# Performance work log

Hardware: AMD Instinct MI355X
Metric: run time of the kernel (lower is better)

## Reference

```python
import jax, jax.numpy as jnp
import numpy as np

N = 50000      # nodes
E = 200000     # edges
IN = 768       # in_dim
HID = 256      # hidden_dim
OUT = 64       # out_dim
H = 4          # heads in conv1
R = 6          # n_relations
NEG = 0.2      # LeakyReLU negative slope (PyG default)
EPS = 1e-5     # LayerNorm eps


def layer_norm(h, g, b):
    mu = jnp.mean(h, axis=-1, keepdims=True)
    var = jnp.mean((h - mu) ** 2, axis=-1, keepdims=True)
    return (h - mu) * jax.lax.rsqrt(var + EPS) * g + b


def gat_layer(x, src, dst, W, a_src, a_dst, bias, heads, dh):
    # project: [N, heads, dh]
    h = (x @ W).reshape(-1, heads, dh)
    # per-node attention logits [N, heads]
    al_s = jnp.sum(h * a_src, axis=-1)
    al_d = jnp.sum(h * a_dst, axis=-1)
    # per-edge scores (edge j->i: source contributes al_s[j], target al_d[i])
    e = jax.nn.leaky_relu(al_s[src] + al_d[dst], NEG)  # [E, heads]
    # segment softmax over edges sharing the same destination node
    e_max = jax.ops.segment_max(e, dst, num_segments=N)        # [N, heads]
    ex = jnp.exp(e - e_max[dst])                               # [E, heads]
    denom = jax.ops.segment_sum(ex, dst, num_segments=N)       # [N, heads]
    alpha = ex / denom[dst]                                    # [E, heads]
    # weighted scatter-aggregate of source messages
    msg = h[src] * alpha[:, :, None]                            # [E, heads, dh]
    out = jax.ops.segment_sum(msg, dst, num_segments=N)        # [N, heads, dh]
    return out.reshape(-1, heads * dh) + bias


def setup_inputs() -> dict:
    key = jax.random.key(0)
    ks = jax.random.split(key, 16)
    s = 0.05  # keep attention logits tame
    return {
        "x": jax.random.normal(ks[0], (N, IN), jnp.float32),
        "edge_index": jax.random.randint(ks[1], (2, E), 0, N, dtype=jnp.int64),
        "edge_type": jax.random.randint(ks[2], (E,), 0, R, dtype=jnp.int64),
        "edge_emb": jax.random.normal(ks[3], (R, IN), jnp.float32) * s,
        "W1": jax.random.normal(ks[4], (IN, H * (HID // H)), jnp.float32) * s,
        "a_src1": jax.random.normal(ks[5], (H, HID // H), jnp.float32) * s,
        "a_dst1": jax.random.normal(ks[6], (H, HID // H), jnp.float32) * s,
        "b1": jnp.zeros((HID,), jnp.float32),
        "g1": jnp.ones((HID,), jnp.float32),
        "be1": jnp.zeros((HID,), jnp.float32),
        "W2": jax.random.normal(ks[7], (HID, OUT), jnp.float32) * s,
        "a_src2": jax.random.normal(ks[8], (1, OUT), jnp.float32) * s,
        "a_dst2": jax.random.normal(ks[9], (1, OUT), jnp.float32) * s,
        "b2": jnp.zeros((OUT,), jnp.float32),
        "g2": jnp.ones((OUT,), jnp.float32),
        "be2": jnp.zeros((OUT,), jnp.float32),
    }


def reference(x, edge_index, edge_type, edge_emb, W1, a_src1, a_dst1, b1, g1, be1,
              W2, a_src2, a_dst2, b2, g2, be2):
    src, dst = edge_index[0], edge_index[1]
    edge_feat = edge_emb[edge_type]                 # [E, IN]
    x_mod = x.at[src].set(x[src] + edge_feat)
    h = gat_layer(x_mod, src, dst, W1, a_src1, a_dst1, b1, H, HID // H)
    h = layer_norm(h, g1, be1)
    h = jax.nn.elu(h)                                # dropout off (inference)
    h = gat_layer(h, src, dst, W2, a_src2, a_dst2, b2, 1, OUT)
    h = layer_norm(h, g2, be2)
    return h
```

## Files before the change

kernel.cpp:

```cpp
#include <hip/hip_runtime.h>
#include <cstdint>
#include <cstddef>

#define NN 50000
#define NE 200000
#define IND 768
#define HID 256
#define OUTD 64
#define NB 196

typedef __bf16 bf16;
typedef __bf16 bf16x8 __attribute__((ext_vector_type(8)));
typedef __bf16 bf16x4 __attribute__((ext_vector_type(4)));
typedef float f32x4 __attribute__((ext_vector_type(4)));

__global__ __launch_bounds__(256) void k_edge_prep(const int* __restrict__ ei,
                                                   int* __restrict__ le, int* __restrict__ deg) {
  int e = blockIdx.x * 256 + threadIdx.x;
  if (e < NE) {
    atomicMax(&le[ei[e]], e);
    atomicAdd(&deg[ei[NE + e]], 1);
  }
}

__global__ __launch_bounds__(256) void k_eembz(const float* __restrict__ eemb,
                                               float* __restrict__ ez) {
  int i = blockIdx.x * 256 + threadIdx.x;
  if (i < 7 * IND) ez[i] = (i < 6 * IND) ? eemb[i] : 0.f;
}

__global__ __launch_bounds__(256) void k_prep_a(const float* __restrict__ x,
                                                const int* __restrict__ le,
                                                const int* __restrict__ et,
                                                const float* __restrict__ eembz,
                                                bf16* __restrict__ A1) {
  int idx = blockIdx.x * 256 + threadIdx.x;
  if (idx >= NN * (IND / 8)) return;
  int row = idx / (IND / 8);
  int c = (idx - row * (IND / 8)) * 8;
  int l = le[row];
  int e = (l >= 0) ? et[l] : 6;
  const float* px = x + (size_t)row * IND + c;
  const float* pe = eembz + (size_t)e * IND + c;
  float4 v0 = *(const float4*)px, v1 = *(const float4*)(px + 4);
  float4 e0 = *(const float4*)pe, e1 = *(const float4*)(pe + 4);
  bf16x8 o;
  o[0] = (bf16)(v0.x + e0.x); o[1] = (bf16)(v0.y + e0.y);
  o[2] = (bf16)(v0.z + e0.z); o[3] = (bf16)(v0.w + e0.w);
  o[4] = (bf16)(v1.x + e1.x); o[5] = (bf16)(v1.y + e1.y);
  o[6] = (bf16)(v1.z + e1.z); o[7] = (bf16)(v1.w + e1.w);
  *(bf16x8*)(A1 + (size_t)row * IND + c) = o;
}

__global__ __launch_bounds__(256) void k_scan_block(const int* __restrict__ deg,
                                                    int* __restrict__ excl, int* __restrict__ bsum) {
  __shared__ int sm[256];
  int tid = threadIdx.x;
  int i = blockIdx.x * 256 + tid;
  int v = (i < NN) ? deg[i] : 0;
  sm[tid] = v;
  __syncthreads();
#pragma unroll
  for (int off = 1; off < 256; off <<= 1) {
    int t = (tid >= off) ? sm[tid - off] : 0;
    __syncthreads();
    sm[tid] += t;
    __syncthreads();
  }
  if (i < NN) excl[i] = sm[tid] - v;
  if (tid == 255) bsum[blockIdx.x] = sm[255];
}

__global__ __launch_bounds__(256) void k_scan_partials(const int* __restrict__ bsum,
                                                       int* __restrict__ bbase) {
  __shared__ int sm[256];
  int tid = threadIdx.x;
  int v = (tid < NB) ? bsum[tid] : 0;
  sm[tid] = v;
  __syncthreads();
#pragma unroll
  for (int off = 1; off < 256; off <<= 1) {
    int t = (tid >= off) ? sm[tid - off] : 0;
    __syncthreads();
    sm[tid] += t;
    __syncthreads();
  }
  bbase[tid] = sm[tid] - v;
}

__global__ __launch_bounds__(256) void k_add_base(const int* __restrict__ excl,
                                                  const int* __restrict__ bbase,
                                                  int* __restrict__ rowstart, int* __restrict__ cur) {
  int i = blockIdx.x * 256 + threadIdx.x;
  if (i < NN) {
    int rs = excl[i] + bbase[i >> 8];
    rowstart[i] = rs;
    cur[i] = rs;
  }
}

__global__ __launch_bounds__(256) void k_scatter_csr(const int* __restrict__ ei,
                                                     int* __restrict__ cur, int* __restrict__ csr) {
  int e = blockIdx.x * 256 + threadIdx.x;
  if (e < NE) {
    int d = ei[NE + e];
    int pos = atomicAdd(&cur[d], 1);
    csr[pos] = ei[e];
  }
}

__global__ __launch_bounds__(256) void k_transpose(const float* __restrict__ W,
                                                   bf16* __restrict__ Wt, int K, int NC) {
  int k = blockIdx.x * 256 + threadIdx.x;
  int n = blockIdx.y;
  if (k < K) Wt[n * K + k] = (bf16)W[k * NC + n];
}

__device__ __forceinline__ void gld16(const bf16* g, bf16* l) {
  __builtin_amdgcn_global_load_lds((const __attribute__((address_space(1))) void*)g,
                                   (__attribute__((address_space(3))) void*)l, 16, 0, 0);
}

template <typename OutT, int TN>
__global__ __launch_bounds__(256) void k_gemm_bt(const bf16* __restrict__ A,
                                                 const bf16* __restrict__ Bt,
                                                 OutT* __restrict__ C,
                                                 int M, int K, int NC,
                                                 const float* __restrict__ aS,
                                                 const float* __restrict__ aD,
                                                 float* __restrict__ alS,
                                                 float* __restrict__ alD,
                                                 int alStride) {
  constexpr int MI = (TN == 128) ? 4 : 2;
  constexpr int WROWS = MI * 16;
  __shared__ bf16 As[2][128 * 32];
  __shared__ bf16 Bs[2][TN * 32];
  const int tid = threadIdx.x;
  const int lane = tid & 63;
  const int wave = tid >> 6;
  const int wr = (TN == 128) ? (wave >> 1) : wave;
  const int wc = (TN == 128) ? (wave & 1) : 0;
  const int ln15 = lane & 15, q = lane >> 4;
  const int n0 = blockIdx.x * TN;
  const int m0 = blockIdx.y * 128;

  const int sr = lane >> 2;
  const int scol = (lane & 3) * 8;
  const int gA0 = min(m0 + wave * 32 + sr, M - 1);
  const int gA1 = min(m0 + wave * 32 + 16 + sr, M - 1);
  int gB0, gB1 = 0;
  if constexpr (TN == 128) {
    gB0 = min(n0 + wave * 32 + sr, NC - 1);
    gB1 = min(n0 + wave * 32 + 16 + sr, NC - 1);
  } else {
    gB0 = min(n0 + wave * 16 + sr, NC - 1);
  }

  auto stage = [&](int buf, int kt) {
    gld16(A + (size_t)gA0 * K + kt + scol, &As[buf][(wave * 32) * 32]);
    gld16(A + (size_t)gA1 * K + kt + scol, &As[buf][(wave * 32 + 16) * 32]);
    if constexpr (TN == 128) {
      gld16(Bt + (size_t)gB0 * K + kt + scol, &Bs[buf][(wave * 32) * 32]);
      gld16(Bt + (size_t)gB1 * K + kt + scol, &Bs[buf][(wave * 32 + 16) * 32]);
    } else {
      gld16(Bt + (size_t)gB0 * K + kt + scol, &Bs[buf][(wave * 16) * 32]);
    }
  };

  f32x4 acc[MI][4] = {};

  auto compute = [&](int buf) {
    bf16x8 af[MI], bfr[4];
#pragma unroll
    for (int i = 0; i < MI; i++)
      af[i] = *(const bf16x8*)(&As[buf][(wr * WROWS + i * 16 + ln15) * 32 + q * 8]);
#pragma unroll
    for (int i = 0; i < 4; i++)
      bfr[i] = *(const bf16x8*)(&Bs[buf][(wc * 64 + i * 16 + ln15) * 32 + q * 8]);
#pragma unroll
    for (int mi = 0; mi < MI; mi++)
#pragma unroll
      for (int ni = 0; ni < 4; ni++)
        acc[mi][ni] = __builtin_amdgcn_mfma_f32_16x16x32_bf16(af[mi], bfr[ni], acc[mi][ni], 0, 0, 0);
  };

  const int NT = K >> 5;

  stage(0, 0);
  stage(1, 32);
  int cur = 0;
  for (int t = 0; t < NT; ++t) {
    if (t < NT - 1) {
      if constexpr (TN == 128) asm volatile("s_waitcnt vmcnt(4)" ::: "memory");
      else                     asm volatile("s_waitcnt vmcnt(3)" ::: "memory");
    } else {
      asm volatile("s_waitcnt vmcnt(0)" ::: "memory");
    }
    __builtin_amdgcn_s_barrier();
    compute(cur);
    if (t + 2 < NT) {
      asm volatile("s_waitcnt lgkmcnt(0)" ::: "memory");
      __builtin_amdgcn_s_barrier();
      stage(cur, (t + 2) << 5);
    }
    cur ^= 1;
  }

#pragma unroll
  for (int mi = 0; mi < MI; mi++)
#pragma unroll
    for (int ni = 0; ni < 4; ni++)
#pragma unroll
      for (int r = 0; r < 4; r++) {
        int row = m0 + wr * WROWS + mi * 16 + q * 4 + r;
        int col = n0 + wc * 64 + ni * 16 + ln15;
        if (row < M && col < NC) C[(size_t)row * NC + col] = (OutT)acc[mi][ni][r];
      }

  if (n0 + wc * 64 < NC) {
    const int hd = (n0 + wc * 64) >> 6;
#pragma unroll
    for (int mi = 0; mi < MI; mi++)
#pragma unroll
      for (int r = 0; r < 4; r++) {
        float ps = 0.f, pd = 0.f;
#pragma unroll
        for (int ni = 0; ni < 4; ni++) {
          int col = n0 + wc * 64 + ni * 16 + ln15;
          float w_s = (col < NC) ? aS[col] : 0.f;
          float w_d = (col < NC) ? aD[col] : 0.f;
          ps += acc[mi][ni][r] * w_s;
          pd += acc[mi][ni][r] * w_d;
        }
#pragma unroll
        for (int off = 1; off < 16; off <<= 1) {
          ps += __shfl_xor(ps, off);
          pd += __shfl_xor(pd, off);
        }
        int row = m0 + wr * WROWS + mi * 16 + q * 4 + r;
        if (ln15 == 0 && row < M) {
          alS[row * alStride + hd] = ps;
          alD[row * alStride + hd] = pd;
        }
      }
  }
}

__global__ __launch_bounds__(256) void k_agg_ln1(const int* __restrict__ rowstart,
                                                 const int* __restrict__ deg,
                                                 const int* __restrict__ csr,
                                                 const bf16* __restrict__ h1,
                                                 const float* __restrict__ alS,
                                                 const float* __restrict__ alD,
                                                 const float* __restrict__ b1,
                                                 const float* __restrict__ g1,
                                                 const float* __restrict__ be1,
                                                 bf16* __restrict__ hln) {
  const int n = blockIdx.x * 4 + (threadIdx.x >> 6);
  const int lane = threadIdx.x & 63;
  const int f0 = lane * 4;
  const int hd = lane >> 4;
  int start = rowstart[n], cnt = deg[n];
  float ald = alD[n * 4 + hd];
  float accv0 = 0.f, accv1 = 0.f, accv2 = 0.f, accv3 = 0.f, accw = 0.f;
  for (int j = 0; j < cnt; j++) {
    int s = csr[start + j];
    float logit = alS[s * 4 + hd] + ald;
    logit = logit >= 0.f ? logit : 0.2f * logit;
    float w = __expf(logit);
    bf16x4 hv = *(const bf16x4*)(h1 + (size_t)s * HID + f0);
    accv0 += w * (float)hv[0];
    accv1 += w * (float)hv[1];
    accv2 += w * (float)hv[2];
    accv3 += w * (float)hv[3];
    accw += w;
  }
  float inv = (cnt > 0) ? 1.f / accw : 0.f;
  float4 bv = *(const float4*)(b1 + f0);
  float v0 = accv0 * inv + bv.x;
  float v1 = accv1 * inv + bv.y;
  float v2 = accv2 * inv + bv.z;
  float v3 = accv3 * inv + bv.w;
  float s = v0 + v1 + v2 + v3;
  float ss = v0 * v0 + v1 * v1 + v2 * v2 + v3 * v3;
#pragma unroll
  for (int off = 32; off; off >>= 1) { s += __shfl_xor(s, off); ss += __shfl_xor(ss, off); }
  float mu = s * (1.f / HID);
  float var = ss * (1.f / HID) - mu * mu;
  float rs = rsqrtf(var + 1e-5f);
  float4 gv = *(const float4*)(g1 + f0);
  float4 ev = *(const float4*)(be1 + f0);
  float y0 = (v0 - mu) * rs * gv.x + ev.x;
  float y1 = (v1 - mu) * rs * gv.y + ev.y;
  float y2 = (v2 - mu) * rs * gv.z + ev.z;
  float y3 = (v3 - mu) * rs * gv.w + ev.w;
  y0 = y0 > 0.f ? y0 : __expf(y0) - 1.f;
  y1 = y1 > 0.f ? y1 : __expf(y1) - 1.f;
  y2 = y2 > 0.f ? y2 : __expf(y2) - 1.f;
  y3 = y3 > 0.f ? y3 : __expf(y3) - 1.f;
  bf16x4 o;
  o[0] = (bf16)y0; o[1] = (bf16)y1; o[2] = (bf16)y2; o[3] = (bf16)y3;
  *(bf16x4*)(hln + (size_t)n * HID + f0) = o;
}

__global__ __launch_bounds__(256) void k_agg_ln2(const int* __restrict__ rowstart,
                                                 const int* __restrict__ deg,
                                                 const int* __restrict__ csr,
                                                 const float* __restrict__ h2,
                                                 const float* __restrict__ alS,
                                                 const float* __restrict__ alD,
                                                 const float* __restrict__ b2,
                                                 const float* __restrict__ g2,
                                                 const float* __restrict__ be2,
                                                 float* __restrict__ out) {
  const int n = blockIdx.x * 4 + (threadIdx.x >> 6);
  const int f = threadIdx.x & 63;
  int start = rowstart[n], cnt = deg[n];
  float ald = alD[n];
  float accv = 0.f, accw = 0.f;
  for (int j = 0; j < cnt; j++) {
    int s = csr[start + j];
    float logit = alS[s] + ald;
    logit = logit >= 0.f ? logit : 0.2f * logit;
    float w = __expf(logit);
    accv += w * h2[(size_t)s * OUTD + f];
    accw += w;
  }
  float v = (cnt > 0) ? accv / accw : 0.f;
  v += b2[f];
  float s = v, ss = v * v;
#pragma unroll
  for (int off = 32; off; off >>= 1) { s += __shfl_xor(s, off); ss += __shfl_xor(ss, off); }
  float mu = s * (1.f / OUTD);
  float var = ss * (1.f / OUTD) - mu * mu;
  out[(size_t)n * OUTD + f] = (v - mu) * rsqrtf(var + 1e-5f) * g2[f] + be2[f];
}

extern "C" void kernel_launch(void* const* d_in, const int* in_sizes, int n_in,
                              void* d_out, int out_size, void* d_ws, size_t ws_size,
                              hipStream_t stream) {
  const float* x    = (const float*)d_in[0];
  const int*   ei   = (const int*)d_in[1];
  const int*   et   = (const int*)d_in[2];
  const float* eemb = (const float*)d_in[3];
  const float* W1   = (const float*)d_in[4];
  const float* as1  = (const float*)d_in[5];
  const float* ad1  = (const float*)d_in[6];
  const float* b1   = (const float*)d_in[7];
  const float* g1   = (const float*)d_in[8];
  const float* be1  = (const float*)d_in[9];
  const float* W2   = (const float*)d_in[10];
  const float* as2  = (const float*)d_in[11];
  const float* ad2  = (const float*)d_in[12];
  const float* b2   = (const float*)d_in[13];
  const float* g2   = (const float*)d_in[14];
  const float* be2  = (const float*)d_in[15];
  float* out = (float*)d_out;

  char* base = (char*)d_ws;
  size_t off = 0;
  auto alloc = [&](size_t bytes) -> void* {
    void* p = base + off;
    off = (off + bytes + 255) & ~(size_t)255;
    return p;
  };
  int*   le    = (int*)alloc((size_t)NN * 4);
  int*   deg   = (int*)alloc((size_t)NN * 4);
  int*   excl  = (int*)alloc((size_t)NN * 4);
  int*   bsum  = (int*)alloc(256 * 4);
  int*   bbase = (int*)alloc(256 * 4);
  int*   rowst = (int*)alloc((size_t)NN * 4);
  int*   cur   = (int*)alloc((size_t)NN * 4);
  int*   csr   = (int*)alloc((size_t)NE * 4);
  bf16*  h1    = (bf16*)alloc((size_t)NN * HID * 2);
  float* alS1  = (float*)alloc((size_t)NN * 4 * 4);
  float* alD1  = (float*)alloc((size_t)NN * 4 * 4);
  bf16*  W1t   = (bf16*)alloc((size_t)HID * IND * 2);
  bf16*  W2t   = (bf16*)alloc((size_t)OUTD * HID * 2);
  float* eembz = (float*)alloc((size_t)7 * IND * 4);
  char*  R     = (char*)alloc((size_t)NN * IND * 2);
  bf16*  A1    = (bf16*)R;
  bf16*  hln   = (bf16*)R;
  float* h2    = (float*)(R + (size_t)NN * HID * 2);
  float* alS2  = (float*)(R + (size_t)NN * HID * 2 + (size_t)NN * OUTD * 4);
  float* alD2  = (float*)(R + (size_t)NN * HID * 2 + (size_t)NN * OUTD * 4 + (size_t)NN * 4);

  hipMemsetAsync(le, 0xFF, (size_t)NN * 4, stream);
  hipMemsetAsync(deg, 0, (size_t)NN * 4, stream);

  k_edge_prep<<<(NE + 255) / 256, 256, 0, stream>>>(ei, le, deg);
  k_eembz<<<(7 * IND + 255) / 256, 256, 0, stream>>>(eemb, eembz);
  k_prep_a<<<(NN * (IND / 8) + 255) / 256, 256, 0, stream>>>(x, le, et, eembz, A1);
  k_scan_block<<<NB, 256, 0, stream>>>(deg, excl, bsum);
  k_scan_partials<<<1, 256, 0, stream>>>(bsum, bbase);
  k_add_base<<<NB, 256, 0, stream>>>(excl, bbase, rowst, cur);
  k_scatter_csr<<<(NE + 255) / 256, 256, 0, stream>>>(ei, cur, csr);

  k_transpose<<<dim3(3, HID), 256, 0, stream>>>(W1, W1t, IND, HID);
  k_transpose<<<dim3(1, OUTD), 256, 0, stream>>>(W2, W2t, HID, OUTD);

  k_gemm_bt<bf16, 128><<<dim3(2, (NN + 127) / 128), 256, 0, stream>>>(
      A1, W1t, h1, NN, IND, HID, as1, ad1, alS1, alD1, 4);
  k_agg_ln1<<<NN / 4, 256, 0, stream>>>(rowst, deg, csr, h1, alS1, alD1, b1, g1, be1, hln);

  k_gemm_bt<float, 64><<<dim3(1, (NN + 127) / 128), 256, 0, stream>>>(
      hln, W2t, h2, NN, HID, OUTD, as2, ad2, alS2, alD2, 1);
  k_agg_ln2<<<NN / 4, 256, 0, stream>>>(rowst, deg, csr, h2, alS2, alD2, b2, g2, be2, out);
}
```

Before: 438.0 us.

## Fuse fp32 x load into GEMM1 and fold edge embedding via precomputed eemb@W1

Measured after the change: 563.3 us. +28.6%, slower.

```diff
diff --git a/kernel.cpp b/kernel.cpp
--- a/kernel.cpp
+++ b/kernel.cpp
@@ -14,6 +14,11 @@
 typedef __bf16 bf16x4 __attribute__((ext_vector_type(4)));
 typedef float f32x4 __attribute__((ext_vector_type(4)));
 
+__global__ __launch_bounds__(256) void k_init(int* __restrict__ le, int* __restrict__ deg) {
+  int i = blockIdx.x * 256 + threadIdx.x;
+  if (i < NN) { le[i] = -1; deg[i] = 0; }
+}
+
 __global__ __launch_bounds__(256) void k_edge_prep(const int* __restrict__ ei,
                                                    int* __restrict__ le, int* __restrict__ deg) {
   int e = blockIdx.x * 256 + threadIdx.x;
@@ -23,33 +28,26 @@
   }
 }
 
-__global__ __launch_bounds__(256) void k_eembz(const float* __restrict__ eemb,
-                                               float* __restrict__ ez) {
-  int i = blockIdx.x * 256 + threadIdx.x;
-  if (i < 7 * IND) ez[i] = (i < 6 * IND) ? eemb[i] : 0.f;
-}
-
-__global__ __launch_bounds__(256) void k_prep_a(const float* __restrict__ x,
-                                                const int* __restrict__ le,
-                                                const int* __restrict__ et,
-                                                const float* __restrict__ eembz,
-                                                bf16* __restrict__ A1) {
-  int idx = blockIdx.x * 256 + threadIdx.x;
-  if (idx >= NN * (IND / 8)) return;
-  int row = idx / (IND / 8);
-  int c = (idx - row * (IND / 8)) * 8;
-  int l = le[row];
-  int e = (l >= 0) ? et[l] : 6;
-  const float* px = x + (size_t)row * IND + c;
-  const float* pe = eembz + (size_t)e * IND + c;
-  float4 v0 = *(const float4*)px, v1 = *(const float4*)(px + 4);
-  float4 e0 = *(const float4*)pe, e1 = *(const float4*)(pe + 4);
-  bf16x8 o;
-  o[0] = (bf16)(v0.x + e0.x); o[1] = (bf16)(v0.y + e0.y);
-  o[2] = (bf16)(v0.z + e0.z); o[3] = (bf16)(v0.w + e0.w);
-  o[4] = (bf16)(v1.x + e1.x); o[5] = (bf16)(v1.y + e1.y);
-  o[6] = (bf16)(v1.z + e1.z); o[7] = (bf16)(v1.w + e1.w);
-  *(bf16x8*)(A1 + (size_t)row * IND + c) = o;
+__global__ __launch_bounds__(256) void k_weights(const float* __restrict__ W1,
+                                                 const float* __restrict__ W2,
+                                                 const float* __restrict__ eemb,
+                                                 bf16* __restrict__ W1t,
+                                                 bf16* __restrict__ W2t,
+                                                 float* __restrict__ eW) {
+  int bx = blockIdx.x, by = blockIdx.y, tid = threadIdx.x;
+  if (bx < 3) {
+    int k = bx * 256 + tid;
+    W1t[by * IND + k] = (bf16)W1[(size_t)k * HID + by];
+  } else if (by < OUTD) {
+    W2t[by * HID + tid] = (bf16)W2[(size_t)tid * OUTD + by];
+  } else if (by < OUTD + 7) {
+    int r = by - OUTD;
+    float s = 0.f;
+    if (r < 6) {
+      for (int k = 0; k < IND; ++k) s += eemb[r * IND + k] * W1[(size_t)k * HID + tid];
+    }
+    eW[r * HID + tid] = s;
+  }
 }
 
 __global__ __launch_bounds__(256) void k_scan_block(const int* __restrict__ deg,
@@ -90,12 +88,17 @@
 
 __global__ __launch_bounds__(256) void k_add_base(const int* __restrict__ excl,
                                                   const int* __restrict__ bbase,
-                                                  int* __restrict__ rowstart, int* __restrict__ cur) {
+                                                  int* __restrict__ rowstart, int* __restrict__ cur,
+                                                  const int* __restrict__ le,
+                                                  const int* __restrict__ et,
+                                                  int* __restrict__ eidx) {
   int i = blockIdx.x * 256 + threadIdx.x;
   if (i < NN) {
     int rs = excl[i] + bbase[i >> 8];
     rowstart[i] = rs;
     cur[i] = rs;
+    int l = le[i];
+    eidx[i] = (l >= 0) ? et[l] : 6;
   }
 }
 
@@ -109,20 +112,14 @@
   }
 }
 
-__global__ __launch_bounds__(256) void k_transpose(const float* __restrict__ W,
-                                                   bf16* __restrict__ Wt, int K, int NC) {
-  int k = blockIdx.x * 256 + threadIdx.x;
-  int n = blockIdx.y;
-  if (k < K) Wt[n * K + k] = (bf16)W[k * NC + n];
-}
-
 __device__ __forceinline__ void gld16(const bf16* g, bf16* l) {
   __builtin_amdgcn_global_load_lds((const __attribute__((address_space(1))) void*)g,
                                    (__attribute__((address_space(3))) void*)l, 16, 0, 0);
 }
 
-template <typename OutT, int TN>
+template <typename OutT, int TN, bool FX>
 __global__ __launch_bounds__(256) void k_gemm_bt(const bf16* __restrict__ A,
+                                                 const float* __restrict__ Ax,
                                                  const bf16* __restrict__ Bt,
                                                  OutT* __restrict__ C,
                                                  int M, int K, int NC,
@@ -130,11 +127,14 @@
                                                  const float* __restrict__ aD,
                                                  float* __restrict__ alS,
                                                  float* __restrict__ alD,
-                                                 int alStride) {
+                                                 int alStride,
+                                                 const int* __restrict__ eidx,
+                                                 const float* __restrict__ eW) {
   constexpr int MI = (TN == 128) ? 4 : 2;
   constexpr int WROWS = MI * 16;
-  __shared__ bf16 As[2][128 * 32];
-  __shared__ bf16 Bs[2][TN * 32];
+  constexpr int NBUF = FX ? 2 : 3;
+  __shared__ bf16 As[NBUF][128 * 32];
+  __shared__ bf16 Bs[NBUF][TN * 32];
   const int tid = threadIdx.x;
   const int lane = tid & 63;
   const int wave = tid >> 6;
@@ -156,9 +156,7 @@
     gB0 = min(n0 + wave * 16 + sr, NC - 1);
   }
 
-  auto stage = [&](int buf, int kt) {
-    gld16(A + (size_t)gA0 * K + kt + scol, &As[buf][(wave * 32) * 32]);
-    gld16(A + (size_t)gA1 * K + kt + scol, &As[buf][(wave * 32 + 16) * 32]);
+  auto stageB = [&](int buf, int kt) {
     if constexpr (TN == 128) {
       gld16(Bt + (size_t)gB0 * K + kt + scol, &Bs[buf][(wave * 32) * 32]);
       gld16(Bt + (size_t)gB1 * K + kt + scol, &Bs[buf][(wave * 32 + 16) * 32]);
@@ -186,24 +184,81 @@
 
   const int NT = K >> 5;
 
-  stage(0, 0);
-  stage(1, 32);
-  int cur = 0;
-  for (int t = 0; t < NT; ++t) {
-    if (t < NT - 1) {
-      if constexpr (TN == 128) asm volatile("s_waitcnt vmcnt(4)" ::: "memory");
-      else                     asm volatile("s_waitcnt vmcnt(3)" ::: "memory");
-    } else {
-      asm volatile("s_waitcnt vmcnt(0)" ::: "memory");
+  if constexpr (FX) {
+    const int r0 = tid >> 2;
+    const int ce = (tid & 3) << 3;
+    const int rr0 = min(m0 + r0, M - 1);
+    const int rr1 = min(m0 + 64 + r0, M - 1);
+    const float* pA0 = Ax + (size_t)rr0 * K + ce;
+    const float* pA1 = Ax + (size_t)rr1 * K + ce;
+    struct ARegs { float4 a00, a01, a10, a11; };
+    ARegs s0, s1;
+    auto issueA = [&](ARegs& R, int kt) {
+      R.a00 = *(const float4*)(pA0 + kt);
+      R.a01 = *(const float4*)(pA0 + kt + 4);
+      R.a10 = *(const float4*)(pA1 + kt);
+      R.a11 = *(const float4*)(pA1 + kt + 4);
+    };
+    auto commitA = [&](int buf, const ARegs& R) {
+      bf16x8 v0, v1;
+      v0[0] = (bf16)R.a00.x; v0[1] = (bf16)R.a00.y; v0[2] = (bf16)R.a00.z; v0[3] = (bf16)R.a00.w;
+      v0[4] = (bf16)R.a01.x; v0[5] = (bf16)R.a01.y; v0[6] = (bf16)R.a01.z; v0[7] = (bf16)R.a01.w;
+      v1[0] = (bf16)R.a10.x; v1[1] = (bf16)R.a10.y; v1[2] = (bf16)R.a10.z; v1[3] = (bf16)R.a10.w;
+      v1[4] = (bf16)R.a11.x; v1[5] = (bf16)R.a11.y; v1[6] = (bf16)R.a11.z; v1[7] = (bf16)R.a11.w;
+      *(bf16x8*)(&As[buf][r0 * 32 + ce]) = v0;
+      *(bf16x8*)(&As[buf][(64 + r0) * 32 + ce]) = v1;
+    };
+
+    issueA(s0, 0);
+    stageB(0, 0);
+    issueA(s1, 32);
+    commitA(0, s0);
+    issueA(s0, 64);
+    int cur = 0;
+    for (int t = 0; t < NT; ++t) {
+      if (t == 0)          asm volatile("s_waitcnt vmcnt(8)" ::: "memory");
+      else if (t < NT - 1) asm volatile("s_waitcnt vmcnt(4)" ::: "memory");
+      else                 asm volatile("s_waitcnt vmcnt(0)" ::: "memory");
+      __builtin_amdgcn_s_barrier();
+      int nxt = cur ^ 1;
+      if (t + 1 < NT) {
+        stageB(nxt, (t + 1) << 5);
+        commitA(nxt, ((t + 1) & 1) ? s1 : s0);
+      }
+      if (t + 3 < NT) issueA(((t + 3) & 1) ? s1 : s0, (t + 3) << 5);
+      compute(cur);
+      cur = nxt;
     }
-    __builtin_amdgcn_s_barrier();
-    compute(cur);
-    if (t + 2 < NT) {
-      asm volatile("s_waitcnt lgkmcnt(0)" ::: "memory");
+  } else {
+    auto stageA = [&](int buf, int kt) {
+      gld16(A + (size_t)gA0 * K + kt + scol, &As[buf][(wave * 32) * 32]);
+      gld16(A + (size_t)gA1 * K + kt + scol, &As[buf][(wave * 32 + 16) * 32]);
+    };
+    stageA(0, 0); stageB(0, 0);
+    stageA(1, 32); stageB(1, 32);
+    for (int t = 0; t < NT; ++t) {
+      if (t < NT - 1) asm volatile("s_waitcnt vmcnt(3)" ::: "memory");
+      else            asm volatile("s_waitcnt vmcnt(0)" ::: "memory");
       __builtin_amdgcn_s_barrier();
-      stage(cur, (t + 2) << 5);
+      if (t + 2 < NT) {
+        int b = (t + 2) % 3;
+        stageA(b, (t + 2) << 5); stageB(b, (t + 2) << 5);
+      }
+      compute(t % 3);
     }
-    cur ^= 1;
+  }
+
+  if constexpr (FX) {
+#pragma unroll
+    for (int mi = 0; mi < MI; mi++)
+#pragma unroll
+      for (int r = 0; r < 4; r++) {
+        int row = m0 + wr * WROWS + mi * 16 + q * 4 + r;
+        int e = eidx[min(row, M - 1)];
+        const float* ew = eW + e * HID + n0 + wc * 64 + ln15;
+#pragma unroll
+        for (int ni = 0; ni < 4; ni++) acc[mi][ni][r] += ew[ni * 16];
+      }
   }
 
 #pragma unroll
@@ -371,39 +426,32 @@
   int*   bbase = (int*)alloc(256 * 4);
   int*   rowst = (int*)alloc((size_t)NN * 4);
   int*   cur   = (int*)alloc((size_t)NN * 4);
+  int*   eidx  = (int*)alloc((size_t)NN * 4);
   int*   csr   = (int*)alloc((size_t)NE * 4);
   bf16*  h1    = (bf16*)alloc((size_t)NN * HID * 2);
   float* alS1  = (float*)alloc((size_t)NN * 4 * 4);
   float* alD1  = (float*)alloc((size_t)NN * 4 * 4);
   bf16*  W1t   = (bf16*)alloc((size_t)HID * IND * 2);
   bf16*  W2t   = (bf16*)alloc((size_t)OUTD * HID * 2);
-  float* eembz = (float*)alloc((size_t)7 * IND * 4);
-  char*  R     = (char*)alloc((size_t)NN * IND * 2);
-  bf16*  A1    = (bf16*)R;
-  bf16*  hln   = (bf16*)R;
-  float* h2    = (float*)(R + (size_t)NN * HID * 2);
-  float* alS2  = (float*)(R + (size_t)NN * HID * 2 + (size_t)NN * OUTD * 4);
-  float* alD2  = (float*)(R + (size_t)NN * HID * 2 + (size_t)NN * OUTD * 4 + (size_t)NN * 4);
-
-  hipMemsetAsync(le, 0xFF, (size_t)NN * 4, stream);
-  hipMemsetAsync(deg, 0, (size_t)NN * 4, stream);
-
+  float* eW    = (float*)alloc((size_t)7 * HID * 4);
+  bf16*  hln   = (bf16*)alloc((size_t)NN * HID * 2);
+  float* h2    = (float*)alloc((size_t)NN * OUTD * 4);
+  float* alS2  = (float*)alloc((size_t)NN * 4);
+  float* alD2  = (float*)alloc((size_t)NN * 4);
+
+  k_init<<<NB, 256, 0, stream>>>(le, deg);
   k_edge_prep<<<(NE + 255) / 256, 256, 0, stream>>>(ei, le, deg);
-  k_eembz<<<(7 * IND + 255) / 256, 256, 0, stream>>>(eemb, eembz);
-  k_prep_a<<<(NN * (IND / 8) + 255) / 256, 256, 0, stream>>>(x, le, et, eembz, A1);
+  k_weights<<<dim3(4, 256), 256, 0, stream>>>(W1, W2, eemb, W1t, W2t, eW);
   k_scan_block<<<NB, 256, 0, stream>>>(deg, excl, bsum);
   k_scan_partials<<<1, 256, 0, stream>>>(bsum, bbase);
-  k_add_base<<<NB, 256, 0, stream>>>(excl, bbase, rowst, cur);
+  k_add_base<<<NB, 256, 0, stream>>>(excl, bbase, rowst, cur, le, et, eidx);
   k_scatter_csr<<<(NE + 255) / 256, 256, 0, stream>>>(ei, cur, csr);
 
-  k_transpose<<<dim3(3, HID), 256, 0, stream>>>(W1, W1t, IND, HID);
-  k_transpose<<<dim3(1, OUTD), 256, 0, stream>>>(W2, W2t, HID, OUTD);
-
-  k_gemm_bt<bf16, 128><<<dim3(2, (NN + 127) / 128), 256, 0, stream>>>(
-      A1, W1t, h1, NN, IND, HID, as1, ad1, alS1, alD1, 4);
+  k_gemm_bt<bf16, 128, true><<<dim3(2, (NN + 127) / 128), 256, 0, stream>>>(
+      nullptr, x, W1t, h1, NN, IND, HID, as1, ad1, alS1, alD1, 4, eidx, eW);
   k_agg_ln1<<<NN / 4, 256, 0, stream>>>(rowst, deg, csr, h1, alS1, alD1, b1, g1, be1, hln);
 
-  k_gemm_bt<float, 64><<<dim3(1, (NN + 127) / 128), 256, 0, stream>>>(
-      hln, W2t, h2, NN, HID, OUTD, as2, ad2, alS2, alD2, 1);
+  k_gemm_bt<float, 64, false><<<dim3(1, (NN + 127) / 128), 256, 0, stream>>>(
+      hln, nullptr, W2t, h2, NN, HID, OUTD, as2, ad2, alS2, alD2, 1, nullptr, nullptr);
   k_agg_ln2<<<NN / 4, 256, 0, stream>>>(rowst, deg, csr, h2, alS2, alD2, b2, g2, be2, out);
 }
```

## Fold edge embedding into GEMM epilogue, fuse front kernels, triple-buffer GEMM

Applied to the files above, without the earlier changes.

Result: slower. 450.3 us (+2.8%).

```diff
diff --git a/kernel.cpp b/kernel.cpp
--- a/kernel.cpp
+++ b/kernel.cpp
@@ -8,48 +8,56 @@
 #define HID 256
 #define OUTD 64
 #define NB 196
+#define NEB 782
+#define NWB 1024
+#define NCB 18750
 
 typedef __bf16 bf16;
 typedef __bf16 bf16x8 __attribute__((ext_vector_type(8)));
 typedef __bf16 bf16x4 __attribute__((ext_vector_type(4)));
 typedef float f32x4 __attribute__((ext_vector_type(4)));
 
-__global__ __launch_bounds__(256) void k_edge_prep(const int* __restrict__ ei,
-                                                   int* __restrict__ le, int* __restrict__ deg) {
-  int e = blockIdx.x * 256 + threadIdx.x;
-  if (e < NE) {
-    atomicMax(&le[ei[e]], e);
-    atomicAdd(&deg[ei[NE + e]], 1);
-  }
-}
-
-__global__ __launch_bounds__(256) void k_eembz(const float* __restrict__ eemb,
-                                               float* __restrict__ ez) {
-  int i = blockIdx.x * 256 + threadIdx.x;
-  if (i < 7 * IND) ez[i] = (i < 6 * IND) ? eemb[i] : 0.f;
-}
-
-__global__ __launch_bounds__(256) void k_prep_a(const float* __restrict__ x,
-                                                const int* __restrict__ le,
-                                                const int* __restrict__ et,
-                                                const float* __restrict__ eembz,
-                                                bf16* __restrict__ A1) {
-  int idx = blockIdx.x * 256 + threadIdx.x;
-  if (idx >= NN * (IND / 8)) return;
-  int row = idx / (IND / 8);
-  int c = (idx - row * (IND / 8)) * 8;
-  int l = le[row];
-  int e = (l >= 0) ? et[l] : 6;
-  const float* px = x + (size_t)row * IND + c;
-  const float* pe = eembz + (size_t)e * IND + c;
-  float4 v0 = *(const float4*)px, v1 = *(const float4*)(px + 4);
-  float4 e0 = *(const float4*)pe, e1 = *(const float4*)(pe + 4);
-  bf16x8 o;
-  o[0] = (bf16)(v0.x + e0.x); o[1] = (bf16)(v0.y + e0.y);
-  o[2] = (bf16)(v0.z + e0.z); o[3] = (bf16)(v0.w + e0.w);
-  o[4] = (bf16)(v1.x + e1.x); o[5] = (bf16)(v1.y + e1.y);
-  o[6] = (bf16)(v1.z + e1.z); o[7] = (bf16)(v1.w + e1.w);
-  *(bf16x8*)(A1 + (size_t)row * IND + c) = o;
+__global__ __launch_bounds__(256) void k_front(const int* __restrict__ ei,
+                                               int* __restrict__ le, int* __restrict__ deg,
+                                               const float* __restrict__ x,
+                                               bf16* __restrict__ A1,
+                                               const float* __restrict__ W1,
+                                               const float* __restrict__ W2,
+                                               const float* __restrict__ eemb,
+                                               bf16* __restrict__ W1t,
+                                               bf16* __restrict__ W2t,
+                                               float* __restrict__ eW) {
+  const int bid = blockIdx.x, tid = threadIdx.x;
+  if (bid < NEB) {
+    int e = bid * 256 + tid;
+    if (e < NE) {
+      atomicMax(&le[ei[e]], e);
+      atomicAdd(&deg[ei[NE + e]], 1);
+    }
+  } else if (bid < NEB + NWB) {
+    int wb = bid - NEB, bx = wb >> 8, by = wb & 255;
+    if (bx < 3) {
+      int k = bx * 256 + tid;
+      W1t[by * IND + k] = (bf16)W1[(size_t)k * HID + by];
+    } else if (by < OUTD) {
+      W2t[by * HID + tid] = (bf16)W2[(size_t)tid * OUTD + by];
+    } else if (by < OUTD + 7) {
+      int r = by - OUTD;
+      float s = 0.f;
+      if (r < 6) {
+        for (int k = 0; k < IND; ++k) s += eemb[r * IND + k] * W1[(size_t)k * HID + tid];
+      }
+      eW[r * HID + tid] = s;
+    }
+  } else {
+    size_t idx = (size_t)(bid - NEB - NWB) * 256 + tid;
+    const float* px = x + idx * 8;
+    float4 v0 = *(const float4*)px, v1 = *(const float4*)(px + 4);
+    bf16x8 o;
+    o[0] = (bf16)v0.x; o[1] = (bf16)v0.y; o[2] = (bf16)v0.z; o[3] = (bf16)v0.w;
+    o[4] = (bf16)v1.x; o[5] = (bf16)v1.y; o[6] = (bf16)v1.z; o[7] = (bf16)v1.w;
+    *(bf16x8*)(A1 + idx * 8) = o;
+  }
 }
 
 __global__ __launch_bounds__(256) void k_scan_block(const int* __restrict__ deg,
@@ -90,12 +98,17 @@
 
 __global__ __launch_bounds__(256) void k_add_base(const int* __restrict__ excl,
                                                   const int* __restrict__ bbase,
-                                                  int* __restrict__ rowstart, int* __restrict__ cur) {
+                                                  int* __restrict__ rowstart, int* __restrict__ cur,
+                                                  const int* __restrict__ le,
+                                                  const int* __restrict__ et,
+                                                  int* __restrict__ eidx) {
   int i = blockIdx.x * 256 + threadIdx.x;
   if (i < NN) {
     int rs = excl[i] + bbase[i >> 8];
     rowstart[i] = rs;
     cur[i] = rs;
+    int l = le[i];
+    eidx[i] = (l >= 0) ? et[l] : 6;
   }
 }
 
@@ -109,19 +122,12 @@
   }
 }
 
-__global__ __launch_bounds__(256) void k_transpose(const float* __restrict__ W,
-                                                   bf16* __restrict__ Wt, int K, int NC) {
-  int k = blockIdx.x * 256 + threadIdx.x;
-  int n = blockIdx.y;
-  if (k < K) Wt[n * K + k] = (bf16)W[k * NC + n];
-}
-
 __device__ __forceinline__ void gld16(const bf16* g, bf16* l) {
   __builtin_amdgcn_global_load_lds((const __attribute__((address_space(1))) void*)g,
                                    (__attribute__((address_space(3))) void*)l, 16, 0, 0);
 }
 
-template <typename OutT, int TN>
+template <typename OutT, int TN, bool EW>
 __global__ __launch_bounds__(256) void k_gemm_bt(const bf16* __restrict__ A,
                                                  const bf16* __restrict__ Bt,
                                                  OutT* __restrict__ C,
@@ -130,11 +136,13 @@
                                                  const float* __restrict__ aD,
                                                  float* __restrict__ alS,
                                                  float* __restrict__ alD,
-                                                 int alStride) {
+                                                 int alStride,
+                                                 const int* __restrict__ eidx,
+                                                 const float* __restrict__ eW) {
   constexpr int MI = (TN == 128) ? 4 : 2;
   constexpr int WROWS = MI * 16;
-  __shared__ bf16 As[2][128 * 32];
-  __shared__ bf16 Bs[2][TN * 32];
+  __shared__ bf16 As[3][128 * 32];
+  __shared__ bf16 Bs[3][TN * 32];
   const int tid = threadIdx.x;
   const int lane = tid & 63;
   const int wave = tid >> 6;
@@ -188,22 +196,32 @@
 
   stage(0, 0);
   stage(1, 32);
-  int cur = 0;
   for (int t = 0; t < NT; ++t) {
-    if (t < NT - 1) {
+    if (t + 2 < NT) {
       if constexpr (TN == 128) asm volatile("s_waitcnt vmcnt(4)" ::: "memory");
       else                     asm volatile("s_waitcnt vmcnt(3)" ::: "memory");
     } else {
       asm volatile("s_waitcnt vmcnt(0)" ::: "memory");
     }
+    __builtin_amdgcn_sched_barrier(0);
     __builtin_amdgcn_s_barrier();
-    compute(cur);
-    if (t + 2 < NT) {
-      asm volatile("s_waitcnt lgkmcnt(0)" ::: "memory");
-      __builtin_amdgcn_s_barrier();
-      stage(cur, (t + 2) << 5);
-    }
-    cur ^= 1;
+    if (t + 2 < NT) stage((t + 2) % 3, (t + 2) << 5);
+    compute(t % 3);
+    asm volatile("s_waitcnt lgkmcnt(0)" ::: "memory");
+    __builtin_amdgcn_sched_barrier(0);
+  }
+
+  if constexpr (EW) {
+#pragma unroll
+    for (int mi = 0; mi < MI; mi++)
+#pragma unroll
+      for (int r = 0; r < 4; r++) {
+        int row = m0 + wr * WROWS + mi * 16 + q * 4 + r;
+        int e = eidx[min(row, M - 1)];
+        const float* ew = eW + e * HID + n0 + wc * 64 + ln15;
+#pragma unroll
+        for (int ni = 0; ni < 4; ni++) acc[mi][ni][r] += ew[ni * 16];
+      }
   }
 
 #pragma unroll
@@ -371,13 +389,14 @@
   int*   bbase = (int*)alloc(256 * 4);
   int*   rowst = (int*)alloc((size_t)NN * 4);
   int*   cur   = (int*)alloc((size_t)NN * 4);
+  int*   eidx  = (int*)alloc((size_t)NN * 4);
   int*   csr   = (int*)alloc((size_t)NE * 4);
   bf16*  h1    = (bf16*)alloc((size_t)NN * HID * 2);
   float* alS1  = (float*)alloc((size_t)NN * 4 * 4);
   float* alD1  = (float*)alloc((size_t)NN * 4 * 4);
   bf16*  W1t   = (bf16*)alloc((size_t)HID * IND * 2);
   bf16*  W2t   = (bf16*)alloc((size_t)OUTD * HID * 2);
-  float* eembz = (float*)alloc((size_t)7 * IND * 4);
+  float* eW    = (float*)alloc((size_t)7 * HID * 4);
   char*  R     = (char*)alloc((size_t)NN * IND * 2);
   bf16*  A1    = (bf16*)R;
   bf16*  hln   = (bf16*)R;
@@ -388,22 +407,17 @@
   hipMemsetAsync(le, 0xFF, (size_t)NN * 4, stream);
   hipMemsetAsync(deg, 0, (size_t)NN * 4, stream);
 
-  k_edge_prep<<<(NE + 255) / 256, 256, 0, stream>>>(ei, le, deg);
-  k_eembz<<<(7 * IND + 255) / 256, 256, 0, stream>>>(eemb, eembz);
-  k_prep_a<<<(NN * (IND / 8) + 255) / 256, 256, 0, stream>>>(x, le, et, eembz, A1);
+  k_front<<<NEB + NWB + NCB, 256, 0, stream>>>(ei, le, deg, x, A1, W1, W2, eemb, W1t, W2t, eW);
   k_scan_block<<<NB, 256, 0, stream>>>(deg, excl, bsum);
   k_scan_partials<<<1, 256, 0, stream>>>(bsum, bbase);
-  k_add_base<<<NB, 256, 0, stream>>>(excl, bbase, rowst, cur);
-  k_scatter_csr<<<(NE + 255) / 256, 256, 0, stream>>>(ei, cur, csr);
-
-  k_transpose<<<dim3(3, HID), 256, 0, stream>>>(W1, W1t, IND, HID);
-  k_transpose<<<dim3(1, OUTD), 256, 0, stream>>>(W2, W2t, HID, OUTD);
-
-  k_gemm_bt<bf16, 128><<<dim3(2, (NN + 127) / 128), 256, 0, stream>>>(
-      A1, W1t, h1, NN, IND, HID, as1, ad1, alS1, alD1, 4);
+  k_add_base<<<NB, 256, 0, stream>>>(excl, bbase, rowst, cur, le, et, eidx);
+  k_scatter_csr<<<NEB, 256, 0, stream>>>(ei, cur, csr);
+
+  k_gemm_bt<bf16, 128, true><<<dim3(2, (NN + 127) / 128), 256, 0, stream>>>(
+      A1, W1t, h1, NN, IND, HID, as1, ad1, alS1, alD1, 4, eidx, eW);
   k_agg_ln1<<<NN / 4, 256, 0, stream>>>(rowst, deg, csr, h1, alS1, alD1, b1, g1, be1, hln);
 
-  k_gemm_bt<float, 64><<<dim3(1, (NN + 127) / 128), 256, 0, stream>>>(
-      hln, W2t, h2, NN, HID, OUTD, as2, ad2, alS2, alD2, 1);
+  k_gemm_bt<float, 64, false><<<dim3(1, (NN + 127) / 128), 256, 0, stream>>>(
+      hln, W2t, h2, NN, HID, OUTD, as2, ad2, alS2, alD2, 1, nullptr, nullptr);
   k_agg_ln2<<<NN / 4, 256, 0, stream>>>(rowst, deg, csr, h2, alS2, alD2, b2, g2, be2, out);
 }
```
